# Performance work log

Hardware: AMD Instinct MI355X
Metric: run time of the kernel (lower is better)

The kernel has to match this reference:

```python
import jax, jax.numpy as jnp
import numpy as np

HEADS = 8
DIM_HEAD = 64


def setup_inputs() -> dict:
    key = jax.random.key(0)
    ks = jax.random.split(key, 6)
    dim = 512
    inner = HEADS * DIM_HEAD  # 512
    x = jax.random.normal(ks[0], (4, 4096, dim), dtype=jnp.float32)
    s = 1.0 / np.sqrt(dim)
    Wq = jax.random.normal(ks[1], (dim, inner), dtype=jnp.float32) * s
    Wk = jax.random.normal(ks[2], (dim, inner), dtype=jnp.float32) * s
    Wv = jax.random.normal(ks[3], (dim, inner), dtype=jnp.float32) * s
    Wo = jax.random.normal(ks[4], (inner, dim), dtype=jnp.float32) * (1.0 / np.sqrt(inner))
    bo = jax.random.normal(ks[5], (dim,), dtype=jnp.float32) * 0.01
    return {"x": x, "Wq": Wq, "Wk": Wk, "Wv": Wv, "Wo": Wo, "bo": bo}


def reference(x, Wq, Wk, Wv, Wo, bo):
    b, n, _ = x.shape
    h, d = HEADS, DIM_HEAD
    # project and split heads: [b, h, n, d]
    q = (x @ Wq).reshape(b, n, h, d).transpose(0, 2, 1, 3)
    k = (x @ Wk).reshape(b, n, h, d).transpose(0, 2, 1, 3)
    v = (x @ Wv).reshape(b, n, h, d).transpose(0, 2, 1, 3)
    q = jax.nn.softmax(q, axis=-1)
    k = jax.nn.softmax(k, axis=-1)
    context = jnp.einsum('bhnd,bhne->bhde', k, v)  # small d x d per head
    out = jnp.einsum('bhnd,bhde->bhne', q, context)
    out = out.transpose(0, 2, 1, 3).reshape(b, n, h * d)
    return out @ Wo + bo
```

## Files before the change

### kernel.cpp

```cpp
#include <hip/hip_runtime.h>

typedef unsigned short u16;
typedef unsigned int   u32;
typedef __bf16 bf16x8 __attribute__((ext_vector_type(8)));
typedef float  f32x4  __attribute__((ext_vector_type(4)));
typedef u16    u16x8  __attribute__((ext_vector_type(8)));
typedef u16    u16x4  __attribute__((ext_vector_type(4)));

__device__ __forceinline__ float b2f(u16 h) {
  return __builtin_bit_cast(float, ((u32)h) << 16);
}
__device__ __forceinline__ u16 f2b(float f) {
  u32 u = __builtin_bit_cast(u32, f);
  u32 r = u + 0x7FFFu + ((u >> 16) & 1u);
  return (u16)(r >> 16);
}

#define GLD_AS1(p) ((const __attribute__((address_space(1))) void*)(p))
#define LDS_AS3(p) ((__attribute__((address_space(3))) void*)(p))

__global__ void gemm_qkv_kernel(const u16* __restrict__ A, const u16* __restrict__ Bt,
                                u16* __restrict__ qb, u16* __restrict__ kT,
                                u16* __restrict__ vT) {
  const int K = 512;
  __shared__ u16 smem[2 * 64 * 72];
  u16* As = smem;
  u16* Bs = smem + 128 * 32;
  const int id = blockIdx.x;
  const int tn = id >> 7;
  const int tm = (id & 7) * 16 + ((id >> 3) & 15);
  const int tileN = tn * 128;
  const int tileM = tm * 128;
  const int t = threadIdx.x;
  const int lane = t & 63;
  const int wave = t >> 6;
  const int mbase = (wave >> 1) * 64;
  const int nbase = (wave & 1) * 64;
  const int fm = lane & 15;
  const int kg = lane >> 4;

  f32x4 acc[4][4];
#pragma unroll
  for (int i = 0; i < 4; ++i)
#pragma unroll
    for (int j = 0; j < 4; ++j) acc[i][j] = (f32x4){0.f, 0.f, 0.f, 0.f};

  for (int k0 = 0; k0 < K; k0 += 32) {
#pragma unroll
    for (int p = 0; p < 2; ++p) {
      int c = p * 256 + t;
      int r = c >> 2;
      int g = (c & 3) ^ ((r >> 1) & 3);
      const u16* ga = A + (size_t)(tileM + r) * K + (k0 + g * 8);
      __builtin_amdgcn_global_load_lds(GLD_AS1(ga), LDS_AS3(As + c * 8), 16, 0, 0);
      const u16* gb = Bt + (size_t)(tileN + r) * K + (k0 + g * 8);
      __builtin_amdgcn_global_load_lds(GLD_AS1(gb), LDS_AS3(Bs + c * 8), 16, 0, 0);
    }
    __syncthreads();

    bf16x8 af[4], bfr[4];
#pragma unroll
    for (int mi = 0; mi < 4; ++mi) {
      int m = mbase + mi * 16 + fm;
      int sg = kg ^ ((m >> 1) & 3);
      af[mi] = *(const bf16x8*)(As + m * 32 + sg * 8);
    }
#pragma unroll
    for (int ni = 0; ni < 4; ++ni) {
      int n = nbase + ni * 16 + fm;
      int sg = kg ^ ((n >> 1) & 3);
      bfr[ni] = *(const bf16x8*)(Bs + n * 32 + sg * 8);
    }
#pragma unroll
    for (int mi = 0; mi < 4; ++mi)
#pragma unroll
      for (int ni = 0; ni < 4; ++ni)
        acc[mi][ni] = __builtin_amdgcn_mfma_f32_16x16x32_bf16(af[mi], bfr[ni],
                                                              acc[mi][ni], 0, 0, 0);
    __syncthreads();
  }

  const int rq = lane >> 4;
  const int region = tn >> 2;

  float inv[4][4];
  if (region <= 1) {
#pragma unroll
    for (int mi = 0; mi < 4; ++mi)
#pragma unroll
      for (int ni = 0; ni < 4; ++ni)
#pragma unroll
        for (int reg = 0; reg < 4; ++reg)
          acc[mi][ni][reg] = __expf(acc[mi][ni][reg]);
#pragma unroll
    for (int mi = 0; mi < 4; ++mi)
#pragma unroll
      for (int reg = 0; reg < 4; ++reg) {
        float s = acc[mi][0][reg] + acc[mi][1][reg] + acc[mi][2][reg] + acc[mi][3][reg];
        s += __shfl_xor(s, 1);
        s += __shfl_xor(s, 2);
        s += __shfl_xor(s, 4);
        s += __shfl_xor(s, 8);
        inv[mi][reg] = 1.f / s;
      }
  } else {
#pragma unroll
    for (int mi = 0; mi < 4; ++mi)
#pragma unroll
      for (int reg = 0; reg < 4; ++reg) inv[mi][reg] = 1.f;
  }

  if (region == 0) {
#pragma unroll
    for (int mi = 0; mi < 4; ++mi)
#pragma unroll
      for (int ni = 0; ni < 4; ++ni)
#pragma unroll
        for (int reg = 0; reg < 4; ++reg) {
          int gr = tileM + mbase + mi * 16 + rq * 4 + reg;
          int gc = tileN + nbase + ni * 16 + fm;
          qb[(size_t)gr * 512 + gc] = f2b(acc[mi][ni][reg] * inv[mi][reg]);
        }
  }

  u16* scw = smem + (wave & 1) * (64 * 72);
  u16* base = (region == 1) ? kT : vT;
  const int hd = tileN + nbase - ((region == 1) ? 512 : 1024);
  const int gr0 = tileM + mbase;
  const int bh = (gr0 >> 12) * 8 + (hd >> 6);
  const int n0 = gr0 & 4095;

  auto transpose_store = [&]() {
#pragma unroll
    for (int mi = 0; mi < 4; ++mi)
#pragma unroll
      for (int ni = 0; ni < 4; ++ni) {
        u16x4 o;
#pragma unroll
        for (int reg = 0; reg < 4; ++reg)
          o[reg] = f2b(acc[mi][ni][reg] * inv[mi][reg]);
        *(u16x4*)(scw + (ni * 16 + fm) * 72 + mi * 16 + rq * 4) = o;
      }
#pragma unroll
    for (int i = 0; i < 8; ++i) {
      int row = i * 8 + (lane >> 3);
      int seg = lane & 7;
      u16x8 val = *(const u16x8*)(scw + row * 72 + seg * 8);
      *(u16x8*)(base + ((size_t)bh * 64 + row) * 4096 + n0 + seg * 8) = val;
    }
  };

  if (region != 0 && wave < 2) transpose_store();
  __syncthreads();
  if (region != 0 && wave >= 2) transpose_store();
}

__global__ void gemm_bt_kernel(const u16* __restrict__ A, const u16* __restrict__ Bt,
                               float* __restrict__ Cout, const float* __restrict__ bias,
                               int N, int K) {
  __shared__ u16 As[128 * 32];
  __shared__ u16 Bs[128 * 32];
  const int id = blockIdx.x;
  const int tn = id >> 7;
  const int tm = (id & 7) * 16 + ((id >> 3) & 15);
  const int tileN = tn * 128;
  const int tileM = tm * 128;
  const int t = threadIdx.x;
  const int lane = t & 63;
  const int wave = t >> 6;
  const int mbase = (wave >> 1) * 64;
  const int nbase = (wave & 1) * 64;
  const int fm = lane & 15;
  const int kg = lane >> 4;

  f32x4 acc[4][4];
#pragma unroll
  for (int i = 0; i < 4; ++i)
#pragma unroll
    for (int j = 0; j < 4; ++j) acc[i][j] = (f32x4){0.f, 0.f, 0.f, 0.f};

  for (int k0 = 0; k0 < K; k0 += 32) {
#pragma unroll
    for (int p = 0; p < 2; ++p) {
      int c = p * 256 + t;
      int r = c >> 2;
      int g = (c & 3) ^ ((r >> 1) & 3);
      const u16* ga = A + (size_t)(tileM + r) * K + (k0 + g * 8);
      __builtin_amdgcn_global_load_lds(GLD_AS1(ga), LDS_AS3(As + c * 8), 16, 0, 0);
      const u16* gb = Bt + (size_t)(tileN + r) * K + (k0 + g * 8);
      __builtin_amdgcn_global_load_lds(GLD_AS1(gb), LDS_AS3(Bs + c * 8), 16, 0, 0);
    }
    __syncthreads();

    bf16x8 af[4], bfr[4];
#pragma unroll
    for (int mi = 0; mi < 4; ++mi) {
      int m = mbase + mi * 16 + fm;
      int sg = kg ^ ((m >> 1) & 3);
      af[mi] = *(const bf16x8*)(As + m * 32 + sg * 8);
    }
#pragma unroll
    for (int ni = 0; ni < 4; ++ni) {
      int n = nbase + ni * 16 + fm;
      int sg = kg ^ ((n >> 1) & 3);
      bfr[ni] = *(const bf16x8*)(Bs + n * 32 + sg * 8);
    }
#pragma unroll
    for (int mi = 0; mi < 4; ++mi)
#pragma unroll
      for (int ni = 0; ni < 4; ++ni)
        acc[mi][ni] = __builtin_amdgcn_mfma_f32_16x16x32_bf16(af[mi], bfr[ni],
                                                              acc[mi][ni], 0, 0, 0);
    __syncthreads();
  }

  const int rq = lane >> 4;
#pragma unroll
  for (int mi = 0; mi < 4; ++mi)
#pragma unroll
    for (int ni = 0; ni < 4; ++ni)
#pragma unroll
      for (int reg = 0; reg < 4; ++reg) {
        int gr = tileM + mbase + mi * 16 + rq * 4 + reg;
        int gc = tileN + nbase + ni * 16 + fm;
        Cout[(size_t)gr * N + gc] = acc[mi][ni][reg] + bias[gc];
      }
}

__global__ void prep_all_kernel(const float* __restrict__ x, const float* __restrict__ Wq,
                                const float* __restrict__ Wk, const float* __restrict__ Wv,
                                const float* __restrict__ Wo, u16* __restrict__ xb,
                                u16* __restrict__ Wt, u16* __restrict__ Wot,
                                float* __restrict__ ctxT) {
  __shared__ u16 tr[64 * 72];
  const int id = blockIdx.x;
  const int t = threadIdx.x;

  if (id < 4096) {
    int i = (id * 256 + t) * 8;
    float4 a = *(const float4*)(x + i);
    float4 b = *(const float4*)(x + i + 4);
    u16x8 o;
    o[0] = f2b(a.x); o[1] = f2b(a.y); o[2] = f2b(a.z); o[3] = f2b(a.w);
    o[4] = f2b(b.x); o[5] = f2b(b.y); o[6] = f2b(b.z); o[7] = f2b(b.w);
    *(u16x8*)(xb + i) = o;
    return;
  }
  if (id < 4352) {
    const float* W;
    u16* dst;
    int n0, k0;
    if (id < 4288) {
      int tile = id - 4096;
      n0 = (tile >> 3) * 64;
      k0 = (tile & 7) * 64;
      W = (n0 < 512) ? Wq : ((n0 < 1024) ? Wk : Wv);
      dst = Wt;
    } else {
      int tile = id - 4288;
      n0 = (tile >> 3) * 64;
      k0 = (tile & 7) * 64;
      W = Wo;
      dst = Wot;
    }
    int cin = (n0 & 511);
    int c = t & 63;
    int r0 = t >> 6;
#pragma unroll
    for (int i = 0; i < 16; ++i) {
      int r = r0 * 16 + i;
      tr[c * 72 + r] = f2b(W[(size_t)(k0 + r) * 512 + cin + c]);
    }
    __syncthreads();
#pragma unroll
    for (int j = 0; j < 2; ++j) {
      int idx = j * 256 + t;
      int row = idx >> 3;
      int seg = idx & 7;
      u16x8 val = *(const u16x8*)(tr + row * 72 + seg * 8);
      *(u16x8*)(dst + (size_t)(n0 + row) * 512 + k0 + seg * 8) = val;
    }
    return;
  }
  int z = id - 4352;
  float* p = ctxT + (size_t)z * 16384;
#pragma unroll
  for (int it = 0; it < 16; ++it)
    *(f32x4*)(p + it * 1024 + t * 4) = (f32x4){0.f, 0.f, 0.f, 0.f};
}

__global__ void context_kernel(const u16* __restrict__ kT, const u16* __restrict__ vT,
                               float* __restrict__ ctxT) {
  __shared__ u16 ks_lds[64 * 32];
  __shared__ u16 vs_lds[64 * 32];
  const int bh = blockIdx.x;
  const int s = blockIdx.y;
  const int t = threadIdx.x;
  const int lane = t & 63;
  const int wave = t >> 6;
  const int fm = lane & 15;
  const int kg = lane >> 4;

  const u16* kbase = kT + (size_t)bh * 64 * 4096;
  const u16* vbase = vT + (size_t)bh * 64 * 4096;
  const int r = t >> 2;
  const int slot = t & 3;
  const int g = slot ^ ((r >> 1) & 3);
  const size_t goff = (size_t)r * 4096 + s * 256 + g * 8;

  f32x4 acc[4];
#pragma unroll
  for (int i = 0; i < 4; ++i) acc[i] = (f32x4){0.f, 0.f, 0.f, 0.f};

  for (int ki = 0; ki < 8; ++ki) {
    __builtin_amdgcn_global_load_lds(GLD_AS1(vbase + goff + ki * 32),
                                     LDS_AS3(vs_lds + t * 8), 16, 0, 0);
    __builtin_amdgcn_global_load_lds(GLD_AS1(kbase + goff + ki * 32),
                                     LDS_AS3(ks_lds + t * 8), 16, 0, 0);
    __syncthreads();
    int e = wave * 16 + fm;
    bf16x8 af = *(const bf16x8*)(vs_lds + e * 32 + (kg ^ ((e >> 1) & 3)) * 8);
#pragma unroll
    for (int dt = 0; dt < 4; ++dt) {
      int d = dt * 16 + fm;
      bf16x8 bfr = *(const bf16x8*)(ks_lds + d * 32 + (kg ^ ((d >> 1) & 3)) * 8);
      acc[dt] = __builtin_amdgcn_mfma_f32_16x16x32_bf16(af, bfr, acc[dt], 0, 0, 0);
    }
    __syncthreads();
  }

  const int rq = lane >> 4;
#pragma unroll
  for (int dt = 0; dt < 4; ++dt)
#pragma unroll
    for (int reg = 0; reg < 4; ++reg)
      atomicAdd(ctxT + ((size_t)bh * 64 + wave * 16 + rq * 4 + reg) * 64 + dt * 16 + fm,
                acc[dt][reg]);
}

__global__ void out2_kernel(const u16* __restrict__ qb, const float* __restrict__ ctxT,
                            u16* __restrict__ attn) {
  __shared__ u16 qs[256 * 64];
  const int bh = blockIdx.x;
  const int mc = blockIdx.y;
  const int b = bh >> 3, h = bh & 7;
  const int t = threadIdx.x;
  const int lane = t & 63;
  const int wave = t >> 6;
  const int fm = lane & 15;
  const int kg = lane >> 4;

  const u16* qrow0 = qb + ((size_t)b * 4096 + mc * 256) * 512 + h * 64;
#pragma unroll
  for (int p = 0; p < 8; ++p) {
    int idx = p * 256 + t;
    int row = idx >> 3;
    int slot = idx & 7;
    int g = slot ^ (row & 7);
    __builtin_amdgcn_global_load_lds(GLD_AS1(qrow0 + (size_t)row * 512 + g * 8),
                                     LDS_AS3(qs + idx * 8), 16, 0, 0);
  }

  const float* cb = ctxT + (size_t)bh * 4096;
  bf16x8 bfr[4][2];
#pragma unroll
  for (int et = 0; et < 4; ++et)
#pragma unroll
    for (int ksi = 0; ksi < 2; ++ksi) {
      int e = et * 16 + fm;
      const float* p = cb + e * 64 + ksi * 32 + kg * 8;
      f32x4 lo = *(const f32x4*)p;
      f32x4 hi = *(const f32x4*)(p + 4);
      u16x8 u;
#pragma unroll
      for (int j = 0; j < 4; ++j) { u[j] = f2b(lo[j]); u[j + 4] = f2b(hi[j]); }
      bfr[et][ksi] = __builtin_bit_cast(bf16x8, u);
    }

  __syncthreads();

  f32x4 acc[4][4];
#pragma unroll
  for (int i = 0; i < 4; ++i)
#pragma unroll
    for (int j = 0; j < 4; ++j) acc[i][j] = (f32x4){0.f, 0.f, 0.f, 0.f};

#pragma unroll
  for (int st = 0; st < 4; ++st) {
    int m = wave * 64 + st * 16 + fm;
#pragma unroll
    for (int ksi = 0; ksi < 2; ++ksi) {
      int sl = (ksi * 4 + kg) ^ (m & 7);
      bf16x8 af = *(const bf16x8*)(qs + m * 64 + sl * 8);
#pragma unroll
      for (int et = 0; et < 4; ++et)
        acc[st][et] = __builtin_amdgcn_mfma_f32_16x16x32_bf16(af, bfr[et][ksi],
                                                              acc[st][et], 0, 0, 0);
    }
  }

  const int rq = lane >> 4;
#pragma unroll
  for (int st = 0; st < 4; ++st)
#pragma unroll
    for (int et = 0; et < 4; ++et)
#pragma unroll
      for (int reg = 0; reg < 4; ++reg) {
        int gr = b * 4096 + mc * 256 + wave * 64 + st * 16 + rq * 4 + reg;
        int e = et * 16 + fm;
        attn[(size_t)gr * 512 + h * 64 + e] = f2b(acc[st][et][reg]);
      }
}

extern "C" void kernel_launch(void* const* d_in, const int* in_sizes, int n_in,
                              void* d_out, int out_size, void* d_ws, size_t ws_size,
                              hipStream_t stream) {
  const float* x  = (const float*)d_in[0];
  const float* Wq = (const float*)d_in[1];
  const float* Wk = (const float*)d_in[2];
  const float* Wv = (const float*)d_in[3];
  const float* Wo = (const float*)d_in[4];
  const float* bo = (const float*)d_in[5];

  char* w = (char*)d_ws;
  u16* xb   = (u16*)w;    w += (size_t)16384 * 512 * 2;
  u16* Wt   = (u16*)w;    w += (size_t)1536 * 512 * 2;
  u16* Wot  = (u16*)w;    w += (size_t)512 * 512 * 2;
  u16* qbuf = (u16*)w;    w += (size_t)16384 * 512 * 2;
  u16* kT   = (u16*)w;    w += (size_t)32 * 64 * 4096 * 2;
  u16* vT   = (u16*)w;    w += (size_t)32 * 64 * 4096 * 2;
  float* ctxT = (float*)w; w += (size_t)32 * 64 * 64 * 4;
  u16* attn = (u16*)w;    w += (size_t)16384 * 512 * 2;

  prep_all_kernel<<<4360, 256, 0, stream>>>(x, Wq, Wk, Wv, Wo, xb, Wt, Wot, ctxT);
  gemm_qkv_kernel<<<1536, 256, 0, stream>>>(xb, Wt, qbuf, kT, vT);
  context_kernel<<<dim3(32, 16), 256, 0, stream>>>(kT, vT, ctxT);
  out2_kernel<<<dim3(32, 16), 256, 0, stream>>>(qbuf, ctxT, attn);
  gemm_bt_kernel<<<512, 256, 0, stream>>>(attn, Wot, (float*)d_out, bo, 512, 512);
}
```

Baseline: 165.4 us.

## Fuse q·context and output projection; replace atomic context accumulation with partial reduce

Merges the q×context kernel and the output-projection GEMM into one kernel. Each 128x128 output tile loops over heads, computing q·ctx into LDS and immediately multiplying by the Wo slice, so the bf16 attention intermediate no longer goes to global memory. Context partials are now written per split into a buffer and summed by a small reduce kernel that also converts to bf16. This removes the zeroing pass and the float atomics. In exchange, each output tile recomputes q·ctx for all heads, which costs extra MFMA work, and a kernel launch is added.

New measurement: 183.1 us. +10.7%, slower.

```diff
diff --git a/kernel.cpp b/kernel.cpp
--- a/kernel.cpp
+++ b/kernel.cpp
@@ -155,83 +155,10 @@
   if (region != 0 && wave >= 2) transpose_store();
 }
 
-__global__ void gemm_bt_kernel(const u16* __restrict__ A, const u16* __restrict__ Bt,
-                               float* __restrict__ Cout, const float* __restrict__ bias,
-                               int N, int K) {
-  __shared__ u16 As[128 * 32];
-  __shared__ u16 Bs[128 * 32];
-  const int id = blockIdx.x;
-  const int tn = id >> 7;
-  const int tm = (id & 7) * 16 + ((id >> 3) & 15);
-  const int tileN = tn * 128;
-  const int tileM = tm * 128;
-  const int t = threadIdx.x;
-  const int lane = t & 63;
-  const int wave = t >> 6;
-  const int mbase = (wave >> 1) * 64;
-  const int nbase = (wave & 1) * 64;
-  const int fm = lane & 15;
-  const int kg = lane >> 4;
-
-  f32x4 acc[4][4];
-#pragma unroll
-  for (int i = 0; i < 4; ++i)
-#pragma unroll
-    for (int j = 0; j < 4; ++j) acc[i][j] = (f32x4){0.f, 0.f, 0.f, 0.f};
-
-  for (int k0 = 0; k0 < K; k0 += 32) {
-#pragma unroll
-    for (int p = 0; p < 2; ++p) {
-      int c = p * 256 + t;
-      int r = c >> 2;
-      int g = (c & 3) ^ ((r >> 1) & 3);
-      const u16* ga = A + (size_t)(tileM + r) * K + (k0 + g * 8);
-      __builtin_amdgcn_global_load_lds(GLD_AS1(ga), LDS_AS3(As + c * 8), 16, 0, 0);
-      const u16* gb = Bt + (size_t)(tileN + r) * K + (k0 + g * 8);
-      __builtin_amdgcn_global_load_lds(GLD_AS1(gb), LDS_AS3(Bs + c * 8), 16, 0, 0);
-    }
-    __syncthreads();
-
-    bf16x8 af[4], bfr[4];
-#pragma unroll
-    for (int mi = 0; mi < 4; ++mi) {
-      int m = mbase + mi * 16 + fm;
-      int sg = kg ^ ((m >> 1) & 3);
-      af[mi] = *(const bf16x8*)(As + m * 32 + sg * 8);
-    }
-#pragma unroll
-    for (int ni = 0; ni < 4; ++ni) {
-      int n = nbase + ni * 16 + fm;
-      int sg = kg ^ ((n >> 1) & 3);
-      bfr[ni] = *(const bf16x8*)(Bs + n * 32 + sg * 8);
-    }
-#pragma unroll
-    for (int mi = 0; mi < 4; ++mi)
-#pragma unroll
-      for (int ni = 0; ni < 4; ++ni)
-        acc[mi][ni] = __builtin_amdgcn_mfma_f32_16x16x32_bf16(af[mi], bfr[ni],
-                                                              acc[mi][ni], 0, 0, 0);
-    __syncthreads();
-  }
-
-  const int rq = lane >> 4;
-#pragma unroll
-  for (int mi = 0; mi < 4; ++mi)
-#pragma unroll
-    for (int ni = 0; ni < 4; ++ni)
-#pragma unroll
-      for (int reg = 0; reg < 4; ++reg) {
-        int gr = tileM + mbase + mi * 16 + rq * 4 + reg;
-        int gc = tileN + nbase + ni * 16 + fm;
-        Cout[(size_t)gr * N + gc] = acc[mi][ni][reg] + bias[gc];
-      }
-}
-
 __global__ void prep_all_kernel(const float* __restrict__ x, const float* __restrict__ Wq,
                                 const float* __restrict__ Wk, const float* __restrict__ Wv,
                                 const float* __restrict__ Wo, u16* __restrict__ xb,
-                                u16* __restrict__ Wt, u16* __restrict__ Wot,
-                                float* __restrict__ ctxT) {
+                                u16* __restrict__ Wt, u16* __restrict__ Wot) {
   __shared__ u16 tr[64 * 72];
   const int id = blockIdx.x;
   const int t = threadIdx.x;
@@ -246,51 +173,43 @@
     *(u16x8*)(xb + i) = o;
     return;
   }
-  if (id < 4352) {
-    const float* W;
-    u16* dst;
-    int n0, k0;
-    if (id < 4288) {
-      int tile = id - 4096;
-      n0 = (tile >> 3) * 64;
-      k0 = (tile & 7) * 64;
-      W = (n0 < 512) ? Wq : ((n0 < 1024) ? Wk : Wv);
-      dst = Wt;
-    } else {
-      int tile = id - 4288;
-      n0 = (tile >> 3) * 64;
-      k0 = (tile & 7) * 64;
-      W = Wo;
-      dst = Wot;
-    }
-    int cin = (n0 & 511);
-    int c = t & 63;
-    int r0 = t >> 6;
-#pragma unroll
-    for (int i = 0; i < 16; ++i) {
-      int r = r0 * 16 + i;
-      tr[c * 72 + r] = f2b(W[(size_t)(k0 + r) * 512 + cin + c]);
-    }
-    __syncthreads();
-#pragma unroll
-    for (int j = 0; j < 2; ++j) {
-      int idx = j * 256 + t;
-      int row = idx >> 3;
-      int seg = idx & 7;
-      u16x8 val = *(const u16x8*)(tr + row * 72 + seg * 8);
-      *(u16x8*)(dst + (size_t)(n0 + row) * 512 + k0 + seg * 8) = val;
-    }
-    return;
-  }
-  int z = id - 4352;
-  float* p = ctxT + (size_t)z * 16384;
-#pragma unroll
-  for (int it = 0; it < 16; ++it)
-    *(f32x4*)(p + it * 1024 + t * 4) = (f32x4){0.f, 0.f, 0.f, 0.f};
+  const float* W;
+  u16* dst;
+  int n0, k0;
+  if (id < 4288) {
+    int tile = id - 4096;
+    n0 = (tile >> 3) * 64;
+    k0 = (tile & 7) * 64;
+    W = (n0 < 512) ? Wq : ((n0 < 1024) ? Wk : Wv);
+    dst = Wt;
+  } else {
+    int tile = id - 4288;
+    n0 = (tile >> 3) * 64;
+    k0 = (tile & 7) * 64;
+    W = Wo;
+    dst = Wot;
+  }
+  int cin = (n0 & 511);
+  int c = t & 63;
+  int r0 = t >> 6;
+#pragma unroll
+  for (int i = 0; i < 16; ++i) {
+    int r = r0 * 16 + i;
+    tr[c * 72 + r] = f2b(W[(size_t)(k0 + r) * 512 + cin + c]);
+  }
+  __syncthreads();
+#pragma unroll
+  for (int j = 0; j < 2; ++j) {
+    int idx = j * 256 + t;
+    int row = idx >> 3;
+    int seg = idx & 7;
+    u16x8 val = *(const u16x8*)(tr + row * 72 + seg * 8);
+    *(u16x8*)(dst + (size_t)(n0 + row) * 512 + k0 + seg * 8) = val;
+  }
 }
 
 __global__ void context_kernel(const u16* __restrict__ kT, const u16* __restrict__ vT,
-                               float* __restrict__ ctxT) {
+                               float* __restrict__ ctxp) {
   __shared__ u16 ks_lds[64 * 32];
   __shared__ u16 vs_lds[64 * 32];
   const int bh = blockIdx.x;
@@ -330,85 +249,143 @@
   }
 
   const int rq = lane >> 4;
+  float* cp = ctxp + ((size_t)s * 32 + bh) * 4096;
 #pragma unroll
   for (int dt = 0; dt < 4; ++dt)
 #pragma unroll
     for (int reg = 0; reg < 4; ++reg)
-      atomicAdd(ctxT + ((size_t)bh * 64 + wave * 16 + rq * 4 + reg) * 64 + dt * 16 + fm,
-                acc[dt][reg]);
-}
-
-__global__ void out2_kernel(const u16* __restrict__ qb, const float* __restrict__ ctxT,
-                            u16* __restrict__ attn) {
-  __shared__ u16 qs[256 * 64];
+      cp[(wave * 16 + rq * 4 + reg) * 64 + dt * 16 + fm] = acc[dt][reg];
+}
+
+__global__ void ctx_reduce_kernel(const float* __restrict__ ctxp, u16* __restrict__ ctxb) {
   const int bh = blockIdx.x;
-  const int mc = blockIdx.y;
-  const int b = bh >> 3, h = bh & 7;
+  const int t = threadIdx.x;
+#pragma unroll
+  for (int it = 0; it < 4; ++it) {
+    int idx = it * 1024 + t * 4;
+    f32x4 s = (f32x4){0.f, 0.f, 0.f, 0.f};
+#pragma unroll
+    for (int p = 0; p < 16; ++p)
+      s += *(const f32x4*)(ctxp + ((size_t)p * 32 + bh) * 4096 + idx);
+    u16x4 o;
+#pragma unroll
+    for (int j = 0; j < 4; ++j) o[j] = f2b(s[j]);
+    *(u16x4*)(ctxb + (size_t)bh * 4096 + idx) = o;
+  }
+}
+
+__global__ void out_fused_kernel(const u16* __restrict__ qb, const u16* __restrict__ ctxb,
+                                 const u16* __restrict__ Wot, const float* __restrict__ bias,
+                                 float* __restrict__ out) {
+  __shared__ u16 qs[128 * 64];
+  __shared__ u16 ws[128 * 64];
+  __shared__ u16 ps[128 * 72];
+  const int id = blockIdx.x;
+  const int tn = id >> 7;
+  const int tm = (id & 7) * 16 + ((id >> 3) & 15);
+  const int tileN = tn * 128;
+  const int rowBase = tm * 128;
+  const int b = tm >> 5;
   const int t = threadIdx.x;
   const int lane = t & 63;
   const int wave = t >> 6;
   const int fm = lane & 15;
   const int kg = lane >> 4;
-
-  const u16* qrow0 = qb + ((size_t)b * 4096 + mc * 256) * 512 + h * 64;
-#pragma unroll
-  for (int p = 0; p < 8; ++p) {
-    int idx = p * 256 + t;
-    int row = idx >> 3;
-    int slot = idx & 7;
-    int g = slot ^ (row & 7);
-    __builtin_amdgcn_global_load_lds(GLD_AS1(qrow0 + (size_t)row * 512 + g * 8),
-                                     LDS_AS3(qs + idx * 8), 16, 0, 0);
-  }
-
-  const float* cb = ctxT + (size_t)bh * 4096;
-  bf16x8 bfr[4][2];
-#pragma unroll
-  for (int et = 0; et < 4; ++et)
-#pragma unroll
-    for (int ksi = 0; ksi < 2; ++ksi) {
-      int e = et * 16 + fm;
-      const float* p = cb + e * 64 + ksi * 32 + kg * 8;
-      f32x4 lo = *(const f32x4*)p;
-      f32x4 hi = *(const f32x4*)(p + 4);
-      u16x8 u;
-#pragma unroll
-      for (int j = 0; j < 4; ++j) { u[j] = f2b(lo[j]); u[j + 4] = f2b(hi[j]); }
-      bfr[et][ksi] = __builtin_bit_cast(bf16x8, u);
-    }
-
-  __syncthreads();
-
-  f32x4 acc[4][4];
+  const int rq = lane >> 4;
+  const int mhalf = (wave >> 1) * 64;
+  const int nhalf = (wave & 1) * 64;
+
+  f32x4 oacc[4][4];
 #pragma unroll
   for (int i = 0; i < 4; ++i)
 #pragma unroll
-    for (int j = 0; j < 4; ++j) acc[i][j] = (f32x4){0.f, 0.f, 0.f, 0.f};
-
-#pragma unroll
-  for (int st = 0; st < 4; ++st) {
-    int m = wave * 64 + st * 16 + fm;
-#pragma unroll
-    for (int ksi = 0; ksi < 2; ++ksi) {
-      int sl = (ksi * 4 + kg) ^ (m & 7);
-      bf16x8 af = *(const bf16x8*)(qs + m * 64 + sl * 8);
-#pragma unroll
-      for (int et = 0; et < 4; ++et)
-        acc[st][et] = __builtin_amdgcn_mfma_f32_16x16x32_bf16(af, bfr[et][ksi],
-                                                              acc[st][et], 0, 0, 0);
-    }
-  }
-
-  const int rq = lane >> 4;
-#pragma unroll
-  for (int st = 0; st < 4; ++st)
-#pragma unroll
-    for (int et = 0; et < 4; ++et)
+    for (int j = 0; j < 4; ++j) oacc[i][j] = (f32x4){0.f, 0.f, 0.f, 0.f};
+
+  for (int h = 0; h < 8; ++h) {
+#pragma unroll
+    for (int p = 0; p < 4; ++p) {
+      int idx = p * 256 + t;
+      int row = idx >> 3;
+      int slot = idx & 7;
+      int g = slot ^ (row & 7);
+      __builtin_amdgcn_global_load_lds(
+          GLD_AS1(qb + (size_t)(rowBase + row) * 512 + h * 64 + g * 8),
+          LDS_AS3(qs + idx * 8), 16, 0, 0);
+      __builtin_amdgcn_global_load_lds(
+          GLD_AS1(Wot + (size_t)(tileN + row) * 512 + h * 64 + g * 8),
+          LDS_AS3(ws + idx * 8), 16, 0, 0);
+    }
+    __syncthreads();
+
+    f32x4 pacc[2][4];
+#pragma unroll
+    for (int i = 0; i < 2; ++i)
+#pragma unroll
+      for (int j = 0; j < 4; ++j) pacc[i][j] = (f32x4){0.f, 0.f, 0.f, 0.f};
+    const u16* cb = ctxb + (size_t)(b * 8 + h) * 4096;
+#pragma unroll
+    for (int ks = 0; ks < 2; ++ks) {
+      bf16x8 af[2];
+#pragma unroll
+      for (int mi = 0; mi < 2; ++mi) {
+        int e = (wave >> 1) * 32 + mi * 16 + fm;
+        af[mi] = *(const bf16x8*)(cb + e * 64 + ks * 32 + kg * 8);
+      }
+#pragma unroll
+      for (int ni = 0; ni < 4; ++ni) {
+        int n = nhalf + ni * 16 + fm;
+        int sl = (ks * 4 + kg) ^ (n & 7);
+        bf16x8 bfq = *(const bf16x8*)(qs + n * 64 + sl * 8);
+#pragma unroll
+        for (int mi = 0; mi < 2; ++mi)
+          pacc[mi][ni] = __builtin_amdgcn_mfma_f32_16x16x32_bf16(af[mi], bfq,
+                                                                 pacc[mi][ni], 0, 0, 0);
+      }
+    }
+#pragma unroll
+    for (int mi = 0; mi < 2; ++mi)
+#pragma unroll
+      for (int ni = 0; ni < 4; ++ni) {
+        u16x4 o;
+#pragma unroll
+        for (int reg = 0; reg < 4; ++reg) o[reg] = f2b(pacc[mi][ni][reg]);
+        int n = nhalf + ni * 16 + fm;
+        int e0 = (wave >> 1) * 32 + mi * 16 + rq * 4;
+        *(u16x4*)(ps + n * 72 + e0) = o;
+      }
+    __syncthreads();
+
+#pragma unroll
+    for (int ks = 0; ks < 2; ++ks) {
+      bf16x8 af2[4];
+#pragma unroll
+      for (int mi = 0; mi < 4; ++mi) {
+        int m = mhalf + mi * 16 + fm;
+        af2[mi] = *(const bf16x8*)(ps + m * 72 + ks * 32 + kg * 8);
+      }
+#pragma unroll
+      for (int ni = 0; ni < 4; ++ni) {
+        int n = nhalf + ni * 16 + fm;
+        int sl = (ks * 4 + kg) ^ (n & 7);
+        bf16x8 bfw = *(const bf16x8*)(ws + n * 64 + sl * 8);
+#pragma unroll
+        for (int mi = 0; mi < 4; ++mi)
+          oacc[mi][ni] = __builtin_amdgcn_mfma_f32_16x16x32_bf16(af2[mi], bfw,
+                                                                 oacc[mi][ni], 0, 0, 0);
+      }
+    }
+    __syncthreads();
+  }
+
+#pragma unroll
+  for (int mi = 0; mi < 4; ++mi)
+#pragma unroll
+    for (int ni = 0; ni < 4; ++ni)
 #pragma unroll
       for (int reg = 0; reg < 4; ++reg) {
-        int gr = b * 4096 + mc * 256 + wave * 64 + st * 16 + rq * 4 + reg;
-        int e = et * 16 + fm;
-        attn[(size_t)gr * 512 + h * 64 + e] = f2b(acc[st][et][reg]);
+        int gr = rowBase + mhalf + mi * 16 + rq * 4 + reg;
+        int gc = tileN + nhalf + ni * 16 + fm;
+        out[(size_t)gr * 512 + gc] = oacc[mi][ni][reg] + bias[gc];
       }
 }
 
@@ -429,12 +406,12 @@
   u16* qbuf = (u16*)w;    w += (size_t)16384 * 512 * 2;
   u16* kT   = (u16*)w;    w += (size_t)32 * 64 * 4096 * 2;
   u16* vT   = (u16*)w;    w += (size_t)32 * 64 * 4096 * 2;
-  float* ctxT = (float*)w; w += (size_t)32 * 64 * 64 * 4;
-  u16* attn = (u16*)w;    w += (size_t)16384 * 512 * 2;
-
-  prep_all_kernel<<<4360, 256, 0, stream>>>(x, Wq, Wk, Wv, Wo, xb, Wt, Wot, ctxT);
+  float* ctxp = (float*)w; w += (size_t)16 * 32 * 4096 * 4;
+  u16* ctxb = (u16*)w;    w += (size_t)32 * 4096 * 2;
+
+  prep_all_kernel<<<4352, 256, 0, stream>>>(x, Wq, Wk, Wv, Wo, xb, Wt, Wot);
   gemm_qkv_kernel<<<1536, 256, 0, stream>>>(xb, Wt, qbuf, kT, vT);
-  context_kernel<<<dim3(32, 16), 256, 0, stream>>>(kT, vT, ctxT);
-  out2_kernel<<<dim3(32, 16), 256, 0, stream>>>(qbuf, ctxT, attn);
-  gemm_bt_kernel<<<512, 256, 0, stream>>>(attn, Wot, (float*)d_out, bo, 512, 512);
-}
+  context_kernel<<<dim3(32, 16), 256, 0, stream>>>(kT, vT, ctxp);
+  ctx_reduce_kernel<<<32, 256, 0, stream>>>(ctxp, ctxb);
+  out_fused_kernel<<<512, 256, 0, stream>>>(qbuf, ctxb, Wot, bo, (float*)d_out);
+}
```

## Fold per-head context into output projection, replacing atomics with partial sums

Applied to the files above, without the earlier changes.

Reassociates the computation so that each batch's output weight is premultiplied by the block-diagonal per-head context matrices (M_b = blockdiag(ctx) · Wo). The final GEMM can then consume q directly, and the q·context kernel and the intermediate attention buffer are removed. Context accumulation now writes 16 split-K partial buffers that a small kernel reduces, instead of issuing float atomics into a zero-initialised buffer, so the zeroing blocks in prep are also dropped. In exchange, the product ctx·Wo is rounded to bf16 an extra time, and a low-parallelism 32-block kernel is added.

Measured after the change: 172.7 us. 1.04x slower.

```diff
diff --git a/kernel.cpp b/kernel.cpp
--- a/kernel.cpp
+++ b/kernel.cpp
@@ -155,83 +155,10 @@
   if (region != 0 && wave >= 2) transpose_store();
 }
 
-__global__ void gemm_bt_kernel(const u16* __restrict__ A, const u16* __restrict__ Bt,
-                               float* __restrict__ Cout, const float* __restrict__ bias,
-                               int N, int K) {
-  __shared__ u16 As[128 * 32];
-  __shared__ u16 Bs[128 * 32];
-  const int id = blockIdx.x;
-  const int tn = id >> 7;
-  const int tm = (id & 7) * 16 + ((id >> 3) & 15);
-  const int tileN = tn * 128;
-  const int tileM = tm * 128;
-  const int t = threadIdx.x;
-  const int lane = t & 63;
-  const int wave = t >> 6;
-  const int mbase = (wave >> 1) * 64;
-  const int nbase = (wave & 1) * 64;
-  const int fm = lane & 15;
-  const int kg = lane >> 4;
-
-  f32x4 acc[4][4];
-#pragma unroll
-  for (int i = 0; i < 4; ++i)
-#pragma unroll
-    for (int j = 0; j < 4; ++j) acc[i][j] = (f32x4){0.f, 0.f, 0.f, 0.f};
-
-  for (int k0 = 0; k0 < K; k0 += 32) {
-#pragma unroll
-    for (int p = 0; p < 2; ++p) {
-      int c = p * 256 + t;
-      int r = c >> 2;
-      int g = (c & 3) ^ ((r >> 1) & 3);
-      const u16* ga = A + (size_t)(tileM + r) * K + (k0 + g * 8);
-      __builtin_amdgcn_global_load_lds(GLD_AS1(ga), LDS_AS3(As + c * 8), 16, 0, 0);
-      const u16* gb = Bt + (size_t)(tileN + r) * K + (k0 + g * 8);
-      __builtin_amdgcn_global_load_lds(GLD_AS1(gb), LDS_AS3(Bs + c * 8), 16, 0, 0);
-    }
-    __syncthreads();
-
-    bf16x8 af[4], bfr[4];
-#pragma unroll
-    for (int mi = 0; mi < 4; ++mi) {
-      int m = mbase + mi * 16 + fm;
-      int sg = kg ^ ((m >> 1) & 3);
-      af[mi] = *(const bf16x8*)(As + m * 32 + sg * 8);
-    }
-#pragma unroll
-    for (int ni = 0; ni < 4; ++ni) {
-      int n = nbase + ni * 16 + fm;
-      int sg = kg ^ ((n >> 1) & 3);
-      bfr[ni] = *(const bf16x8*)(Bs + n * 32 + sg * 8);
-    }
-#pragma unroll
-    for (int mi = 0; mi < 4; ++mi)
-#pragma unroll
-      for (int ni = 0; ni < 4; ++ni)
-        acc[mi][ni] = __builtin_amdgcn_mfma_f32_16x16x32_bf16(af[mi], bfr[ni],
-                                                              acc[mi][ni], 0, 0, 0);
-    __syncthreads();
-  }
-
-  const int rq = lane >> 4;
-#pragma unroll
-  for (int mi = 0; mi < 4; ++mi)
-#pragma unroll
-    for (int ni = 0; ni < 4; ++ni)
-#pragma unroll
-      for (int reg = 0; reg < 4; ++reg) {
-        int gr = tileM + mbase + mi * 16 + rq * 4 + reg;
-        int gc = tileN + nbase + ni * 16 + fm;
-        Cout[(size_t)gr * N + gc] = acc[mi][ni][reg] + bias[gc];
-      }
-}
-
 __global__ void prep_all_kernel(const float* __restrict__ x, const float* __restrict__ Wq,
                                 const float* __restrict__ Wk, const float* __restrict__ Wv,
                                 const float* __restrict__ Wo, u16* __restrict__ xb,
-                                u16* __restrict__ Wt, u16* __restrict__ Wot,
-                                float* __restrict__ ctxT) {
+                                u16* __restrict__ Wt, u16* __restrict__ Wot) {
   __shared__ u16 tr[64 * 72];
   const int id = blockIdx.x;
   const int t = threadIdx.x;
@@ -246,51 +173,43 @@
     *(u16x8*)(xb + i) = o;
     return;
   }
-  if (id < 4352) {
-    const float* W;
-    u16* dst;
-    int n0, k0;
-    if (id < 4288) {
-      int tile = id - 4096;
-      n0 = (tile >> 3) * 64;
-      k0 = (tile & 7) * 64;
-      W = (n0 < 512) ? Wq : ((n0 < 1024) ? Wk : Wv);
-      dst = Wt;
-    } else {
-      int tile = id - 4288;
-      n0 = (tile >> 3) * 64;
-      k0 = (tile & 7) * 64;
-      W = Wo;
-      dst = Wot;
-    }
-    int cin = (n0 & 511);
-    int c = t & 63;
-    int r0 = t >> 6;
-#pragma unroll
-    for (int i = 0; i < 16; ++i) {
-      int r = r0 * 16 + i;
-      tr[c * 72 + r] = f2b(W[(size_t)(k0 + r) * 512 + cin + c]);
-    }
-    __syncthreads();
-#pragma unroll
-    for (int j = 0; j < 2; ++j) {
-      int idx = j * 256 + t;
-      int row = idx >> 3;
-      int seg = idx & 7;
-      u16x8 val = *(const u16x8*)(tr + row * 72 + seg * 8);
-      *(u16x8*)(dst + (size_t)(n0 + row) * 512 + k0 + seg * 8) = val;
-    }
-    return;
-  }
-  int z = id - 4352;
-  float* p = ctxT + (size_t)z * 16384;
-#pragma unroll
-  for (int it = 0; it < 16; ++it)
-    *(f32x4*)(p + it * 1024 + t * 4) = (f32x4){0.f, 0.f, 0.f, 0.f};
+  const float* W;
+  u16* dst;
+  int n0, k0;
+  if (id < 4288) {
+    int tile = id - 4096;
+    n0 = (tile >> 3) * 64;
+    k0 = (tile & 7) * 64;
+    W = (n0 < 512) ? Wq : ((n0 < 1024) ? Wk : Wv);
+    dst = Wt;
+  } else {
+    int tile = id - 4288;
+    n0 = (tile >> 3) * 64;
+    k0 = (tile & 7) * 64;
+    W = Wo;
+    dst = Wot;
+  }
+  int cin = (n0 & 511);
+  int c = t & 63;
+  int r0 = t >> 6;
+#pragma unroll
+  for (int i = 0; i < 16; ++i) {
+    int r = r0 * 16 + i;
+    tr[c * 72 + r] = f2b(W[(size_t)(k0 + r) * 512 + cin + c]);
+  }
+  __syncthreads();
+#pragma unroll
+  for (int j = 0; j < 2; ++j) {
+    int idx = j * 256 + t;
+    int row = idx >> 3;
+    int seg = idx & 7;
+    u16x8 val = *(const u16x8*)(tr + row * 72 + seg * 8);
+    *(u16x8*)(dst + (size_t)(n0 + row) * 512 + k0 + seg * 8) = val;
+  }
 }
 
 __global__ void context_kernel(const u16* __restrict__ kT, const u16* __restrict__ vT,
-                               float* __restrict__ ctxT) {
+                               float* __restrict__ ctxp) {
   __shared__ u16 ks_lds[64 * 32];
   __shared__ u16 vs_lds[64 * 32];
   const int bh = blockIdx.x;
@@ -318,97 +237,158 @@
     __builtin_amdgcn_global_load_lds(GLD_AS1(kbase + goff + ki * 32),
                                      LDS_AS3(ks_lds + t * 8), 16, 0, 0);
     __syncthreads();
-    int e = wave * 16 + fm;
-    bf16x8 af = *(const bf16x8*)(vs_lds + e * 32 + (kg ^ ((e >> 1) & 3)) * 8);
-#pragma unroll
-    for (int dt = 0; dt < 4; ++dt) {
-      int d = dt * 16 + fm;
-      bf16x8 bfr = *(const bf16x8*)(ks_lds + d * 32 + (kg ^ ((d >> 1) & 3)) * 8);
-      acc[dt] = __builtin_amdgcn_mfma_f32_16x16x32_bf16(af, bfr, acc[dt], 0, 0, 0);
+    int d = wave * 16 + fm;
+    bf16x8 af = *(const bf16x8*)(ks_lds + d * 32 + (kg ^ ((d >> 1) & 3)) * 8);
+#pragma unroll
+    for (int et = 0; et < 4; ++et) {
+      int e = et * 16 + fm;
+      bf16x8 bfr = *(const bf16x8*)(vs_lds + e * 32 + (kg ^ ((e >> 1) & 3)) * 8);
+      acc[et] = __builtin_amdgcn_mfma_f32_16x16x32_bf16(af, bfr, acc[et], 0, 0, 0);
     }
     __syncthreads();
   }
 
   const int rq = lane >> 4;
-#pragma unroll
-  for (int dt = 0; dt < 4; ++dt)
+  float* cp = ctxp + ((size_t)s * 32 + bh) * 4096;
+#pragma unroll
+  for (int et = 0; et < 4; ++et)
 #pragma unroll
     for (int reg = 0; reg < 4; ++reg)
-      atomicAdd(ctxT + ((size_t)bh * 64 + wave * 16 + rq * 4 + reg) * 64 + dt * 16 + fm,
-                acc[dt][reg]);
-}
-
-__global__ void out2_kernel(const u16* __restrict__ qb, const float* __restrict__ ctxT,
-                            u16* __restrict__ attn) {
-  __shared__ u16 qs[256 * 64];
+      cp[(wave * 16 + rq * 4 + reg) * 64 + et * 16 + fm] = acc[et][reg];
+}
+
+__global__ void ctxm_kernel(const float* __restrict__ ctxp, const u16* __restrict__ Wot,
+                            u16* __restrict__ Mt) {
+  __shared__ u16 ctxd[64 * 72];
   const int bh = blockIdx.x;
-  const int mc = blockIdx.y;
   const int b = bh >> 3, h = bh & 7;
   const int t = threadIdx.x;
   const int lane = t & 63;
   const int wave = t >> 6;
   const int fm = lane & 15;
   const int kg = lane >> 4;
-
-  const u16* qrow0 = qb + ((size_t)b * 4096 + mc * 256) * 512 + h * 64;
-#pragma unroll
-  for (int p = 0; p < 8; ++p) {
-    int idx = p * 256 + t;
-    int row = idx >> 3;
-    int slot = idx & 7;
-    int g = slot ^ (row & 7);
-    __builtin_amdgcn_global_load_lds(GLD_AS1(qrow0 + (size_t)row * 512 + g * 8),
-                                     LDS_AS3(qs + idx * 8), 16, 0, 0);
-  }
-
-  const float* cb = ctxT + (size_t)bh * 4096;
-  bf16x8 bfr[4][2];
-#pragma unroll
-  for (int et = 0; et < 4; ++et)
-#pragma unroll
-    for (int ksi = 0; ksi < 2; ++ksi) {
-      int e = et * 16 + fm;
-      const float* p = cb + e * 64 + ksi * 32 + kg * 8;
-      f32x4 lo = *(const f32x4*)p;
-      f32x4 hi = *(const f32x4*)(p + 4);
-      u16x8 u;
-#pragma unroll
-      for (int j = 0; j < 4; ++j) { u[j] = f2b(lo[j]); u[j + 4] = f2b(hi[j]); }
-      bfr[et][ksi] = __builtin_bit_cast(bf16x8, u);
-    }
-
+  const int rq = lane >> 4;
+
+#pragma unroll
+  for (int it = 0; it < 4; ++it) {
+    int idx = it * 1024 + t * 4;
+    f32x4 s = (f32x4){0.f, 0.f, 0.f, 0.f};
+#pragma unroll
+    for (int p = 0; p < 16; ++p)
+      s += *(const f32x4*)(ctxp + ((size_t)p * 32 + bh) * 4096 + idx);
+    u16x4 o;
+#pragma unroll
+    for (int j = 0; j < 4; ++j) o[j] = f2b(s[j]);
+    int d = idx >> 6, e = idx & 63;
+    *(u16x4*)(ctxd + d * 72 + e) = o;
+  }
   __syncthreads();
 
+  f32x4 acc[8][4];
+#pragma unroll
+  for (int i = 0; i < 8; ++i)
+#pragma unroll
+    for (int j = 0; j < 4; ++j) acc[i][j] = (f32x4){0.f, 0.f, 0.f, 0.f};
+
+#pragma unroll
+  for (int ks = 0; ks < 2; ++ks) {
+    bf16x8 bfr[4];
+#pragma unroll
+    for (int dt = 0; dt < 4; ++dt)
+      bfr[dt] = *(const bf16x8*)(ctxd + (dt * 16 + fm) * 72 + ks * 32 + kg * 8);
+#pragma unroll
+    for (int mi = 0; mi < 8; ++mi) {
+      int c = wave * 128 + mi * 16 + fm;
+      bf16x8 af = *(const bf16x8*)(Wot + (size_t)c * 512 + h * 64 + ks * 32 + kg * 8);
+#pragma unroll
+      for (int dt = 0; dt < 4; ++dt)
+        acc[mi][dt] = __builtin_amdgcn_mfma_f32_16x16x32_bf16(af, bfr[dt],
+                                                              acc[mi][dt], 0, 0, 0);
+    }
+  }
+
+  u16* mb = Mt + (size_t)b * 512 * 512;
+#pragma unroll
+  for (int mi = 0; mi < 8; ++mi)
+#pragma unroll
+    for (int dt = 0; dt < 4; ++dt)
+#pragma unroll
+      for (int reg = 0; reg < 4; ++reg) {
+        int c = wave * 128 + mi * 16 + rq * 4 + reg;
+        mb[(size_t)c * 512 + h * 64 + dt * 16 + fm] = f2b(acc[mi][dt][reg]);
+      }
+}
+
+__global__ void gemm_out_kernel(const u16* __restrict__ A, const u16* __restrict__ Mt,
+                                float* __restrict__ Cout, const float* __restrict__ bias) {
+  const int K = 512, N = 512;
+  __shared__ u16 As[128 * 32];
+  __shared__ u16 Bs[128 * 32];
+  const int id = blockIdx.x;
+  const int tn = id >> 7;
+  const int tm = (id & 7) * 16 + ((id >> 3) & 15);
+  const int tileN = tn * 128;
+  const int tileM = tm * 128;
+  const u16* Bt = Mt + (size_t)(tm >> 5) * 512 * 512;
+  const int t = threadIdx.x;
+  const int lane = t & 63;
+  const int wave = t >> 6;
+  const int mbase = (wave >> 1) * 64;
+  const int nbase = (wave & 1) * 64;
+  const int fm = lane & 15;
+  const int kg = lane >> 4;
+
   f32x4 acc[4][4];
 #pragma unroll
   for (int i = 0; i < 4; ++i)
 #pragma unroll
     for (int j = 0; j < 4; ++j) acc[i][j] = (f32x4){0.f, 0.f, 0.f, 0.f};
 
-#pragma unroll
-  for (int st = 0; st < 4; ++st) {
-    int m = wave * 64 + st * 16 + fm;
-#pragma unroll
-    for (int ksi = 0; ksi < 2; ++ksi) {
-      int sl = (ksi * 4 + kg) ^ (m & 7);
-      bf16x8 af = *(const bf16x8*)(qs + m * 64 + sl * 8);
-#pragma unroll
-      for (int et = 0; et < 4; ++et)
-        acc[st][et] = __builtin_amdgcn_mfma_f32_16x16x32_bf16(af, bfr[et][ksi],
-                                                              acc[st][et], 0, 0, 0);
-    }
+  for (int k0 = 0; k0 < K; k0 += 32) {
+#pragma unroll
+    for (int p = 0; p < 2; ++p) {
+      int c = p * 256 + t;
+      int r = c >> 2;
+      int g = (c & 3) ^ ((r >> 1) & 3);
+      const u16* ga = A + (size_t)(tileM + r) * K + (k0 + g * 8);
+      __builtin_amdgcn_global_load_lds(GLD_AS1(ga), LDS_AS3(As + c * 8), 16, 0, 0);
+      const u16* gb = Bt + (size_t)(tileN + r) * K + (k0 + g * 8);
+      __builtin_amdgcn_global_load_lds(GLD_AS1(gb), LDS_AS3(Bs + c * 8), 16, 0, 0);
+    }
+    __syncthreads();
+
+    bf16x8 af[4], bfr[4];
+#pragma unroll
+    for (int mi = 0; mi < 4; ++mi) {
+      int m = mbase + mi * 16 + fm;
+      int sg = kg ^ ((m >> 1) & 3);
+      af[mi] = *(const bf16x8*)(As + m * 32 + sg * 8);
+    }
+#pragma unroll
+    for (int ni = 0; ni < 4; ++ni) {
+      int n = nbase + ni * 16 + fm;
+      int sg = kg ^ ((n >> 1) & 3);
+      bfr[ni] = *(const bf16x8*)(Bs + n * 32 + sg * 8);
+    }
+#pragma unroll
+    for (int mi = 0; mi < 4; ++mi)
+#pragma unroll
+      for (int ni = 0; ni < 4; ++ni)
+        acc[mi][ni] = __builtin_amdgcn_mfma_f32_16x16x32_bf16(af[mi], bfr[ni],
+                                                              acc[mi][ni], 0, 0, 0);
+    __syncthreads();
   }
 
   const int rq = lane >> 4;
 #pragma unroll
-  for (int st = 0; st < 4; ++st)
-#pragma unroll
-    for (int et = 0; et < 4; ++et)
+  for (int mi = 0; mi < 4; ++mi)
+#pragma unroll
+    for (int ni = 0; ni < 4; ++ni)
 #pragma unroll
       for (int reg = 0; reg < 4; ++reg) {
-        int gr = b * 4096 + mc * 256 + wave * 64 + st * 16 + rq * 4 + reg;
-        int e = et * 16 + fm;
-        attn[(size_t)gr * 512 + h * 64 + e] = f2b(acc[st][et][reg]);
+        int gr = tileM + mbase + mi * 16 + rq * 4 + reg;
+        int gc = tileN + nbase + ni * 16 + fm;
+        Cout[(size_t)gr * N + gc] = acc[mi][ni][reg] + bias[gc];
       }
 }
 
@@ -429,12 +409,12 @@
   u16* qbuf = (u16*)w;    w += (size_t)16384 * 512 * 2;
   u16* kT   = (u16*)w;    w += (size_t)32 * 64 * 4096 * 2;
   u16* vT   = (u16*)w;    w += (size_t)32 * 64 * 4096 * 2;
-  float* ctxT = (float*)w; w += (size_t)32 * 64 * 64 * 4;
-  u16* attn = (u16*)w;    w += (size_t)16384 * 512 * 2;
-
-  prep_all_kernel<<<4360, 256, 0, stream>>>(x, Wq, Wk, Wv, Wo, xb, Wt, Wot, ctxT);
+  float* ctxp = (float*)w; w += (size_t)16 * 32 * 4096 * 4;
+  u16* Mt   = (u16*)w;    w += (size_t)4 * 512 * 512 * 2;
+
+  prep_all_kernel<<<4352, 256, 0, stream>>>(x, Wq, Wk, Wv, Wo, xb, Wt, Wot);
   gemm_qkv_kernel<<<1536, 256, 0, stream>>>(xb, Wt, qbuf, kT, vT);
-  context_kernel<<<dim3(32, 16), 256, 0, stream>>>(kT, vT, ctxT);
-  out2_kernel<<<dim3(32, 16), 256, 0, stream>>>(qbuf, ctxT, attn);
-  gemm_bt_kernel<<<512, 256, 0, stream>>>(attn, Wot, (float*)d_out, bo, 512, 512);
-}
+  context_kernel<<<dim3(32, 16), 256, 0, stream>>>(kT, vT, ctxp);
+  ctxm_kernel<<<32, 256, 0, stream>>>(ctxp, Wot, Mt);
+  gemm_out_kernel<<<512, 256, 0, stream>>>(qbuf, Mt, (float*)d_out, bo);
+}
```
